# Kernel optimization log

Hardware: AMD Instinct MI355X
Metric: run time of the kernel (lower is better)

Reference implementation:

```python
import jax, jax.numpy as jnp
import numpy as np


def setup_inputs() -> dict:
    key = jax.random.key(0)
    k1, k2, k3 = jax.random.split(key, 3)
    B, R, N, A, U = 64, 5, 512, 64, 128
    adjacency = jax.random.uniform(k1, (B, R, N, N), dtype=jnp.float32)
    features = jax.random.normal(k2, (B, N, A), dtype=jnp.float32)
    kernel = jax.random.normal(k3, (R, A, U), dtype=jnp.float32) * 0.05
    bias = jnp.zeros((R, 1, U), dtype=jnp.float32)
    return {"adjacency": adjacency, "features": features, "kernel": kernel, "bias": bias}


def reference(adjacency, features, kernel, bias):
    # adjacency: [B, R, N, N], features: [B, N, A]
    # aggregate neighbourhoods per relation: [B, R, N, A]
    agg = jnp.einsum("brnm,bma->brna", adjacency, features)
    # relation-wise projection: [B, R, N, U]
    dp = jnp.einsum("brna,rau->brnu", agg, kernel) + bias  # bias broadcasts over B, N
    # sum over relation axis, then activation: [B, N, U]
    return jax.nn.relu(jnp.sum(dp, axis=1))
```

## Files before the change

### kernel.cpp

```cpp
#include <hip/hip_runtime.h>
#include <hip/hip_bf16.h>

typedef __attribute__((ext_vector_type(4))) float f32x4;
typedef __attribute__((ext_vector_type(8))) short s16x8;
typedef __attribute__((ext_vector_type(4))) short s16x4;

__device__ __forceinline__ unsigned short f2bf(float f) {
  __hip_bfloat16 h = __float2bfloat16(f);
  return __builtin_bit_cast(unsigned short, h);
}

#define AS1U(p) ((const __attribute__((address_space(1))) unsigned int*)(p))
#define AS3U(p) ((__attribute__((address_space(3))) unsigned int*)(p))

__global__ void k_prep(const float* __restrict__ F, const float* __restrict__ K,
                       const float* __restrict__ bias,
                       unsigned short* __restrict__ FT, unsigned short* __restrict__ KT,
                       float* __restrict__ bsum) {
  __shared__ float t[64][65];
  const int b  = blockIdx.x >> 3;
  const int m0 = (blockIdx.x & 7) * 64;
  const int tid = threadIdx.x;
  {
    const int row = tid >> 2, ac = (tid & 3) * 16;
    const float* src = F + ((size_t)b * 512 + m0 + row) * 64 + ac;
    #pragma unroll
    for (int j = 0; j < 4; ++j) {
      f32x4 v = *(const f32x4*)(src + j * 4);
      t[row][ac + j * 4 + 0] = v[0]; t[row][ac + j * 4 + 1] = v[1];
      t[row][ac + j * 4 + 2] = v[2]; t[row][ac + j * 4 + 3] = v[3];
    }
  }
  if (tid < 80) {
    const int idx = blockIdx.x * 80 + tid;
    const int u = idx / 320, ra = idx % 320;
    KT[idx] = f2bf(K[(size_t)ra * 128 + u]);
  }
  if (blockIdx.x == 0 && tid >= 128 && tid < 256) {
    const int u = tid - 128;
    float s = 0.f;
    #pragma unroll
    for (int r = 0; r < 5; ++r) s += bias[r * 128 + u];
    bsum[u] = s;
  }
  __syncthreads();
  {
    const int a = tid >> 2, mc = (tid & 3) * 16;
    unsigned short* dst = FT + ((size_t)b * 64 + a) * 512 + m0 + mc;
    s16x8 p0, p1;
    #pragma unroll
    for (int j = 0; j < 8; ++j) {
      p0[j] = (short)f2bf(t[mc + j][a]);
      p1[j] = (short)f2bf(t[mc + 8 + j][a]);
    }
    *(s16x8*)(dst) = p0;
    *(s16x8*)(dst + 8) = p1;
  }
}

__global__ __launch_bounds__(256, 2) void k_fused(const float* __restrict__ Adj,
                                                  const unsigned short* __restrict__ FT,
                                                  const unsigned short* __restrict__ KT,
                                                  const float* __restrict__ bsum,
                                                  float* __restrict__ out) {
  __shared__ __align__(16) float shq[4][2][16][128];
  const int b  = blockIdx.x >> 3;
  const int nt = blockIdx.x & 7;
  const int w  = threadIdx.x >> 6;
  const int l  = threadIdx.x & 63;
  const int l15 = l & 15, g = l >> 4;

  const float* adjW = Adj + (size_t)b * 5 * 262144 + (size_t)(nt * 64 + w * 16) * 512;
  const unsigned short* ftW = FT + (size_t)b * 64 * 512;
  const int srow = l >> 5;
  const int c16  = (l & 31) * 16;

  float* qw = &shq[w][0][0][0];

  #pragma unroll
  for (int i = 0; i < 8; ++i) {
    const int xr = (2 * i) & 7;
    const float* src = adjW + (size_t)(2 * i + srow) * 512 + ((c16 ^ ((xr + srow) << 4)) >> 2);
    __builtin_amdgcn_global_load_lds(AS1U(src), AS3U(qw + i * 256), 16, 0, 0);
  }

  f32x4 acc[5][4];
  #pragma unroll
  for (int r = 0; r < 5; ++r)
    #pragma unroll
    for (int at = 0; at < 4; ++at) acc[r][at] = (f32x4)0.f;

  #pragma unroll
  for (int ks4 = 0; ks4 < 4; ++ks4) {
    s16x8 ffrag[4][4];
    #pragma unroll
    for (int ksl = 0; ksl < 4; ++ksl)
      #pragma unroll
      for (int at = 0; at < 4; ++at)
        ffrag[ksl][at] = *(const s16x8*)(ftW + (size_t)(at * 16 + l15) * 512 + ks4 * 128 + ksl * 32 + g * 8);

    #pragma unroll
    for (int r = 0; r < 5; ++r) {
      const int s = ks4 * 5 + r;
      const int cur = s & 1;
      const bool have_next = (s < 19);
      if (have_next) {
        const int rn = (r == 4) ? 0 : r + 1;
        const int kn = (r == 4) ? ks4 + 1 : ks4;
        const float* sb = adjW + (size_t)rn * 262144 + kn * 128;
        #pragma unroll
        for (int i = 0; i < 8; ++i) {
          const int xr = (2 * i) & 7;
          const float* src = sb + (size_t)(2 * i + srow) * 512 + ((c16 ^ ((xr + srow) << 4)) >> 2);
          __builtin_amdgcn_global_load_lds(AS1U(src), AS3U(qw + (cur ^ 1) * 2048 + i * 256), 16, 0, 0);
        }
        asm volatile("s_waitcnt vmcnt(8)" ::: "memory");
      } else {
        asm volatile("s_waitcnt vmcnt(0)" ::: "memory");
      }
      __builtin_amdgcn_sched_barrier(0);

      const char* qr = (const char*)(qw + cur * 2048 + l15 * 128);
      const int x = (l15 & 7) << 4;
      #pragma unroll
      for (int ksl = 0; ksl < 4; ++ksl) {
        const int C = ksl * 128 + g * 32;
        f32x4 lo = *(const f32x4*)(qr + (C ^ x));
        f32x4 hi = *(const f32x4*)(qr + ((C + 16) ^ x));
        s16x8 bfrag;
        #pragma unroll
        for (int j = 0; j < 4; ++j) {
          bfrag[j]     = (short)f2bf(lo[j]);
          bfrag[4 + j] = (short)f2bf(hi[j]);
        }
        acc[r][0] = __builtin_amdgcn_mfma_f32_16x16x32_bf16(ffrag[ksl][0], bfrag, acc[r][0], 0, 0, 0);
        acc[r][1] = __builtin_amdgcn_mfma_f32_16x16x32_bf16(ffrag[ksl][1], bfrag, acc[r][1], 0, 0, 0);
        acc[r][2] = __builtin_amdgcn_mfma_f32_16x16x32_bf16(ffrag[ksl][2], bfrag, acc[r][2], 0, 0, 0);
        acc[r][3] = __builtin_amdgcn_mfma_f32_16x16x32_bf16(ffrag[ksl][3], bfrag, acc[r][3], 0, 0, 0);
      }
    }
  }

  unsigned short* agw = (unsigned short*)qw;
  #pragma unroll
  for (int r = 0; r < 5; ++r)
    #pragma unroll
    for (int at = 0; at < 4; ++at) {
      s16x4 pk;
      pk[0] = (short)f2bf(acc[r][at][0]); pk[1] = (short)f2bf(acc[r][at][1]);
      pk[2] = (short)f2bf(acc[r][at][2]); pk[3] = (short)f2bf(acc[r][at][3]);
      *(s16x4*)&agw[l15 * 328 + r * 64 + at * 16 + g * 4] = pk;
    }

  f32x4 o[8];
  #pragma unroll
  for (int ut = 0; ut < 8; ++ut) o[ut] = (f32x4)0.f;

  #pragma unroll 2
  for (int ks = 0; ks < 10; ++ks) {
    s16x8 af = *(const s16x8*)&agw[l15 * 328 + ks * 32 + g * 8];
    #pragma unroll
    for (int ut = 0; ut < 8; ++ut) {
      s16x8 kf = *(const s16x8*)(KT + (size_t)(ut * 16 + l15) * 320 + ks * 32 + g * 8);
      o[ut] = __builtin_amdgcn_mfma_f32_16x16x32_bf16(af, kf, o[ut], 0, 0, 0);
    }
  }

  #pragma unroll
  for (int ut = 0; ut < 8; ++ut) {
    const int u = ut * 16 + l15;
    const float bs = bsum[u];
    float* op = out + ((size_t)b * 512 + nt * 64 + w * 16 + g * 4) * 128 + u;
    #pragma unroll
    for (int t = 0; t < 4; ++t) {
      float vv = o[ut][t] + bs;
      op[(size_t)t * 128] = vv > 0.f ? vv : 0.f;
    }
  }
}

extern "C" void kernel_launch(void* const* d_in, const int* in_sizes, int n_in,
                              void* d_out, int out_size, void* d_ws, size_t ws_size,
                              hipStream_t stream) {
  const float* adj  = (const float*)d_in[0];
  const float* feat = (const float*)d_in[1];
  const float* kern = (const float*)d_in[2];
  const float* bias = (const float*)d_in[3];
  float* out = (float*)d_out;

  char* ws = (char*)d_ws;
  unsigned short* FT   = (unsigned short*)ws;
  unsigned short* KT   = (unsigned short*)(ws + 4194304);
  float*          bsum = (float*)(ws + 4194304 + 81920);

  hipLaunchKernelGGL(k_prep,  dim3(512), dim3(256), 0, stream, feat, kern, bias, FT, KT, bsum);
  hipLaunchKernelGGL(k_fused, dim3(512), dim3(256), 0, stream, adj, FT, KT, bsum, out);
  (void)in_sizes; (void)n_in; (void)out_size; (void)ws_size;
}
```

Before: 89.18 us.

## Use triple-buffered smaller adjacency stages to raise occupancy to three blocks

Each wave's adjacency staging tile shrinks from 16x128 to 16x64 floats, and the double buffer becomes a triple buffer that prefetches two stages ahead. LDS per wave drops from 16KB to 12KB, with the aggregate buffer unioned into the same space. Launch bounds are raised to allow three blocks per CU. The aim is more loads in flight and better latency hiding. In exchange there are twice as many pipeline steps with their waitcnt barriers, and register pressure tightens under the higher occupancy target.

```diff
diff --git a/kernel.cpp b/kernel.cpp
--- a/kernel.cpp
+++ b/kernel.cpp
@@ -58,12 +58,17 @@
   }
 }
 
-__global__ __launch_bounds__(256, 2) void k_fused(const float* __restrict__ Adj,
+union WaveMem {
+  float q[3][16][64];
+  unsigned short ag[16][328];
+};
+
+__global__ __launch_bounds__(256, 3) void k_fused(const float* __restrict__ Adj,
                                                   const unsigned short* __restrict__ FT,
                                                   const unsigned short* __restrict__ KT,
                                                   const float* __restrict__ bsum,
                                                   float* __restrict__ out) {
-  __shared__ __align__(16) float shq[4][2][16][128];
+  __shared__ __align__(16) WaveMem shm[4];
   const int b  = blockIdx.x >> 3;
   const int nt = blockIdx.x & 7;
   const int w  = threadIdx.x >> 6;
@@ -72,17 +77,28 @@
 
   const float* adjW = Adj + (size_t)b * 5 * 262144 + (size_t)(nt * 64 + w * 16) * 512;
   const unsigned short* ftW = FT + (size_t)b * 64 * 512;
-  const int srow = l >> 5;
-  const int c16  = (l & 31) * 16;
-
-  float* qw = &shq[w][0][0][0];
-
-  #pragma unroll
-  for (int i = 0; i < 8; ++i) {
-    const int xr = (2 * i) & 7;
-    const float* src = adjW + (size_t)(2 * i + srow) * 512 + ((c16 ^ ((xr + srow) << 4)) >> 2);
-    __builtin_amdgcn_global_load_lds(AS1U(src), AS3U(qw + i * 256), 16, 0, 0);
-  }
+  const int srow4 = l >> 4;
+  const int scolb = (l & 15) * 16;
+  const int cswz0 = (scolb ^ ((srow4 + 0) << 4)) >> 2;
+  const int cswz1 = (scolb ^ ((srow4 + 4) << 4)) >> 2;
+
+  float* qb = &shm[w].q[0][0][0];
+
+#define ISSUE_STAGE(rn, kn, bn)                                                    \
+  {                                                                                \
+    const float* sb_ = adjW + (size_t)(rn) * 262144 + (kn) * 64;                   \
+    __builtin_amdgcn_global_load_lds(AS1U(sb_ + (size_t)(0 + srow4) * 512 + cswz0), \
+                                     AS3U(qb + (bn) * 1024 + 0 * 256), 16, 0, 0);  \
+    __builtin_amdgcn_global_load_lds(AS1U(sb_ + (size_t)(4 + srow4) * 512 + cswz1), \
+                                     AS3U(qb + (bn) * 1024 + 1 * 256), 16, 0, 0);  \
+    __builtin_amdgcn_global_load_lds(AS1U(sb_ + (size_t)(8 + srow4) * 512 + cswz0), \
+                                     AS3U(qb + (bn) * 1024 + 2 * 256), 16, 0, 0);  \
+    __builtin_amdgcn_global_load_lds(AS1U(sb_ + (size_t)(12 + srow4) * 512 + cswz1),\
+                                     AS3U(qb + (bn) * 1024 + 3 * 256), 16, 0, 0);  \
+  }
+
+  ISSUE_STAGE(0, 0, 0);
+  ISSUE_STAGE(1, 0, 1);
 
   f32x4 acc[5][4];
   #pragma unroll
@@ -90,43 +106,40 @@
     #pragma unroll
     for (int at = 0; at < 4; ++at) acc[r][at] = (f32x4)0.f;
 
-  #pragma unroll
-  for (int ks4 = 0; ks4 < 4; ++ks4) {
-    s16x8 ffrag[4][4];
-    #pragma unroll
-    for (int ksl = 0; ksl < 4; ++ksl)
+  const int xrd = (l15 & 7) << 4;
+
+  #pragma unroll
+  for (int kc4 = 0; kc4 < 8; ++kc4) {
+    s16x8 ffrag[2][4];
+    #pragma unroll
+    for (int ksl = 0; ksl < 2; ++ksl)
       #pragma unroll
       for (int at = 0; at < 4; ++at)
-        ffrag[ksl][at] = *(const s16x8*)(ftW + (size_t)(at * 16 + l15) * 512 + ks4 * 128 + ksl * 32 + g * 8);
+        ffrag[ksl][at] = *(const s16x8*)(ftW + (size_t)(at * 16 + l15) * 512 + kc4 * 64 + ksl * 32 + g * 8);
 
     #pragma unroll
     for (int r = 0; r < 5; ++r) {
-      const int s = ks4 * 5 + r;
-      const int cur = s & 1;
-      const bool have_next = (s < 19);
-      if (have_next) {
-        const int rn = (r == 4) ? 0 : r + 1;
-        const int kn = (r == 4) ? ks4 + 1 : ks4;
-        const float* sb = adjW + (size_t)rn * 262144 + kn * 128;
-        #pragma unroll
-        for (int i = 0; i < 8; ++i) {
-          const int xr = (2 * i) & 7;
-          const float* src = sb + (size_t)(2 * i + srow) * 512 + ((c16 ^ ((xr + srow) << 4)) >> 2);
-          __builtin_amdgcn_global_load_lds(AS1U(src), AS3U(qw + (cur ^ 1) * 2048 + i * 256), 16, 0, 0);
-        }
+      const int s = kc4 * 5 + r;
+      const int cur = s % 3;
+      if (s + 2 <= 39) {
+        const int sn = s + 2;
+        ISSUE_STAGE(sn % 5, sn / 5, sn % 3);
+      }
+      if (s <= 37) {
         asm volatile("s_waitcnt vmcnt(8)" ::: "memory");
+      } else if (s == 38) {
+        asm volatile("s_waitcnt vmcnt(4)" ::: "memory");
       } else {
         asm volatile("s_waitcnt vmcnt(0)" ::: "memory");
       }
       __builtin_amdgcn_sched_barrier(0);
 
-      const char* qr = (const char*)(qw + cur * 2048 + l15 * 128);
-      const int x = (l15 & 7) << 4;
+      const char* qr = (const char*)(qb + cur * 1024 + l15 * 64);
       #pragma unroll
-      for (int ksl = 0; ksl < 4; ++ksl) {
+      for (int ksl = 0; ksl < 2; ++ksl) {
         const int C = ksl * 128 + g * 32;
-        f32x4 lo = *(const f32x4*)(qr + (C ^ x));
-        f32x4 hi = *(const f32x4*)(qr + ((C + 16) ^ x));
+        f32x4 lo = *(const f32x4*)(qr + (C ^ xrd));
+        f32x4 hi = *(const f32x4*)(qr + ((C + 16) ^ xrd));
         s16x8 bfrag;
         #pragma unroll
         for (int j = 0; j < 4; ++j) {
@@ -140,8 +153,9 @@
       }
     }
   }
-
-  unsigned short* agw = (unsigned short*)qw;
+#undef ISSUE_STAGE
+
+  unsigned short* agw = shm[w].ag[0];
   #pragma unroll
   for (int r = 0; r < 5; ++r)
     #pragma unroll
```

Result: slower. 102.2 us (+14.6%).
